# Kernel optimization log

Measured on AMD Instinct MI355X. Metric: run time of the kernel, lower is better.

## Reference

```python
import jax, jax.numpy as jnp
import numpy as np

N, E, D, A = 50000, 800000, 128, 5


def _glorot(key, shape):
    fan = shape[0] + shape[1]
    s = jnp.sqrt(6.0 / fan)
    return jax.random.uniform(key, shape, jnp.float32, -s, s)


def setup_inputs() -> dict:
    key = jax.random.key(0)
    ks = jax.random.split(key, 16)
    x = jax.random.normal(ks[0], (N, D), jnp.float32)
    edge_index = jax.random.randint(ks[1], (2, E), 0, N, jnp.int32)
    return {
        "x": x,
        "anchor_node": _glorot(ks[2], (A, D)),          # NodePromptplus.anchor_prompt
        "attn_w": _glorot(ks[3], (D, A)),               # NodePromptplus.attention (in,out)
        "attn_b": jnp.zeros((A,), jnp.float32),
        "anchor_edge": _glorot(ks[4], (A, D)),          # EdgePromptplus.anchor_prompt
        "w_w": _glorot(ks[5], (2 * D, A)),              # EdgePromptplus.w[0]
        "w_b": jnp.zeros((A,), jnp.float32),
        "cd1_w": _glorot(ks[6], (2 * D, D)),            # causal_discovery Linear1
        "cd1_b": jnp.zeros((D,), jnp.float32),
        "cd2_w": _glorot(ks[7], (D, D)),                # causal_discovery Linear2
        "cd2_b": jnp.zeros((D,), jnp.float32),
        "int_w": _glorot(ks[8], (D, D)),                # intervention Linear
        "int_b": jnp.zeros((D,), jnp.float32),
        "edge_index": edge_index,
        "layer": 0,
    }


def reference(x, anchor_node, attn_w, attn_b, anchor_edge, w_w, w_b,
              cd1_w, cd1_b, cd2_w, cd2_b, int_w, int_b, edge_index, layer):
    # --- NodePromptplus.add ---
    w = jax.nn.softmax(x @ attn_w + attn_b, axis=1)            # [N,A]
    node_px = x + w @ anchor_node                              # [N,D]
    # --- EdgePromptplus.get_prompt ---
    src, dst = edge_index[0], edge_index[1]
    combined_x = jnp.concatenate([x[src], x[dst]], axis=1)     # [E,2D]
    b = jax.nn.softmax(jax.nn.leaky_relu(combined_x @ w_w + w_b), axis=1)  # [E,A]
    edge_prompt = b @ anchor_edge                              # [E,D]
    # --- index_add scatter to both endpoints ---
    agg = jnp.zeros_like(x).at[src].add(edge_prompt).at[dst].add(edge_prompt)
    # --- causal discovery gating + intervention ---
    combined = jnp.concatenate([node_px, agg], axis=1)         # [N,2D]
    h = jax.nn.relu(combined @ cd1_w + cd1_b)
    causal_strength = jax.nn.sigmoid(h @ cd2_w + cd2_b)        # [N,D]
    intervened = (node_px + agg) @ int_w + int_b               # [N,D]
    final_x = node_px + causal_strength * intervened
    return final_x, edge_prompt
```

## Files before the change

### kernel.cpp

```cpp
#include <hip/hip_runtime.h>
#include <math.h>

#define D 128
#define A 5
#define TM 64
#define CSTR 68

__global__ __launch_bounds__(256) void node_prompt_kernel(
    const float* __restrict__ x,
    const float* __restrict__ attn_w, const float* __restrict__ attn_b,
    const float* __restrict__ anchor_node,
    const float* __restrict__ w_w,
    float* __restrict__ node_px,
    float* __restrict__ lsrc, float* __restrict__ ldst, int N)
{
    int t = threadIdx.x;
    int lane = t & 63;
    int j = lane * 2;
    float At0[A], At1[A], AN0[A], AN1[A], Ab[A];
    float W0[A], W1[A], W2[A], W3[A];
    #pragma unroll
    for (int a = 0; a < A; a++) {
        At0[a] = attn_w[(size_t)j * A + a];
        At1[a] = attn_w[(size_t)(j + 1) * A + a];
        AN0[a] = anchor_node[a * D + j];
        AN1[a] = anchor_node[a * D + j + 1];
        Ab[a]  = attn_b[a];
        W0[a]  = w_w[(size_t)j * A + a];
        W1[a]  = w_w[(size_t)(j + 1) * A + a];
        W2[a]  = w_w[(size_t)(D + j) * A + a];
        W3[a]  = w_w[(size_t)(D + j + 1) * A + a];
    }
    int wid = blockIdx.x * 4 + (t >> 6);
    int nw  = gridDim.x * 4;
    for (int n = wid; n < N; n += nw) {
        float2 xv = *(const float2*)&x[(size_t)n * D + j];
        float l[A], es[A], ed[A];
        #pragma unroll
        for (int a = 0; a < A; a++) {
            float p0 = xv.x * At0[a] + xv.y * At1[a];
            float p1 = xv.x * W0[a]  + xv.y * W1[a];
            float p2 = xv.x * W2[a]  + xv.y * W3[a];
            #pragma unroll
            for (int off = 32; off; off >>= 1) {
                p0 += __shfl_xor(p0, off);
                p1 += __shfl_xor(p1, off);
                p2 += __shfl_xor(p2, off);
            }
            l[a]  = p0 + Ab[a];
            es[a] = p1;
            ed[a] = p2;
        }
        float m = l[0];
        #pragma unroll
        for (int a = 1; a < A; a++) m = fmaxf(m, l[a]);
        float s = 0.f;
        #pragma unroll
        for (int a = 0; a < A; a++) { l[a] = __expf(l[a] - m); s += l[a]; }
        float inv = 1.f / s;
        float2 o = xv;
        #pragma unroll
        for (int a = 0; a < A; a++) {
            float w = l[a] * inv;
            o.x += w * AN0[a];
            o.y += w * AN1[a];
        }
        *(float2*)&node_px[(size_t)n * D + j] = o;
        if (lane < A) {
            float vs = es[0], vd = ed[0];
            #pragma unroll
            for (int a = 1; a < A; a++) if (lane == a) { vs = es[a]; vd = ed[a]; }
            lsrc[(size_t)n * A + lane] = vs;
            ldst[(size_t)n * A + lane] = vd;
        }
    }
}

__global__ __launch_bounds__(256) void edge_kernel(
    const int* __restrict__ ei,
    const float* __restrict__ lsrc, const float* __restrict__ ldst,
    const float* __restrict__ w_b, const float* __restrict__ anchor_edge,
    float* __restrict__ edge_prompt, float* __restrict__ bagg, int E)
{
    int t = threadIdx.x;
    int lane = t & 63;
    int j = lane * 2;
    float AE0[A], AE1[A], Wb[A];
    #pragma unroll
    for (int a = 0; a < A; a++) {
        AE0[a] = anchor_edge[a * D + j];
        AE1[a] = anchor_edge[a * D + j + 1];
        Wb[a]  = w_b[a];
    }
    int sub  = lane & 31;
    int half = lane >> 5;
    int wid = blockIdx.x * 4 + (t >> 6);
    int nw  = gridDim.x * 4;
    #pragma unroll 2
    for (int e = wid; e < E; e += nw) {
        int s = __builtin_amdgcn_readfirstlane(ei[e]);
        int d = __builtin_amdgcn_readfirstlane(ei[(size_t)E + e]);
        const float* ps = &lsrc[(size_t)s * A];
        const float* pd = &ldst[(size_t)d * A];
        float l[A];
        #pragma unroll
        for (int a = 0; a < A; a++) {
            float p = ps[a] + pd[a] + Wb[a];
            l[a] = (p > 0.f) ? p : 0.01f * p;
        }
        float m = l[0];
        #pragma unroll
        for (int a = 1; a < A; a++) m = fmaxf(m, l[a]);
        float sum = 0.f;
        #pragma unroll
        for (int a = 0; a < A; a++) { l[a] = __expf(l[a] - m); sum += l[a]; }
        float inv = 1.f / sum;
        float2 ep = make_float2(0.f, 0.f);
        #pragma unroll
        for (int a = 0; a < A; a++) {
            float b = l[a] * inv;
            ep.x += b * AE0[a];
            ep.y += b * AE1[a];
        }
        *(float2*)&edge_prompt[(size_t)e * D + j] = ep;
        if (sub < A) {
            float bv = l[0];
            #pragma unroll
            for (int a = 1; a < A; a++) if (sub == a) bv = l[a];
            bv *= inv;
            int node = half ? d : s;
            atomicAdd(&bagg[(size_t)node * A + sub], bv);
        }
    }
}

__global__ __launch_bounds__(256) void agg_kernel(
    const float* __restrict__ bagg, const float* __restrict__ anchor_edge,
    float* __restrict__ agg, int N)
{
    __shared__ float AE[A * D];
    int t = threadIdx.x;
    for (int f = t; f < A * D; f += 256) AE[f] = anchor_edge[f];
    __syncthreads();
    int total = N * (D / 4);
    for (int i = blockIdx.x * 256 + t; i < total; i += gridDim.x * 256) {
        int n = i >> 5;
        int c = (i & 31) * 4;
        const float* br = &bagg[(size_t)n * A];
        float b0 = br[0], b1 = br[1], b2 = br[2], b3 = br[3], b4 = br[4];
        float4 e0 = *(float4*)&AE[0 * D + c];
        float4 e1 = *(float4*)&AE[1 * D + c];
        float4 e2 = *(float4*)&AE[2 * D + c];
        float4 e3 = *(float4*)&AE[3 * D + c];
        float4 e4 = *(float4*)&AE[4 * D + c];
        float4 r;
        r.x = b0 * e0.x + b1 * e1.x + b2 * e2.x + b3 * e3.x + b4 * e4.x;
        r.y = b0 * e0.y + b1 * e1.y + b2 * e2.y + b3 * e3.y + b4 * e4.y;
        r.z = b0 * e0.z + b1 * e1.z + b2 * e2.z + b3 * e3.z + b4 * e4.z;
        r.w = b0 * e0.w + b1 * e1.w + b2 * e2.w + b3 * e3.w + b4 * e4.w;
        *(float4*)&agg[(size_t)n * D + c] = r;
    }
}

__device__ __forceinline__ void fma4(float4& acc, const float4 cv,
                                     const float4 w0, const float4 w1,
                                     const float4 w2, const float4 w3)
{
    acc.x += cv.x * w0.x + cv.y * w1.x + cv.z * w2.x + cv.w * w3.x;
    acc.y += cv.x * w0.y + cv.y * w1.y + cv.z * w2.y + cv.w * w3.y;
    acc.z += cv.x * w0.z + cv.y * w1.z + cv.z * w2.z + cv.w * w3.z;
    acc.w += cv.x * w0.w + cv.y * w1.w + cv.z * w2.w + cv.w * w3.w;
}

__global__ __launch_bounds__(256) void cd1_kernel(
    const float* __restrict__ node_px, const float* __restrict__ agg,
    const float* __restrict__ cd1_w, const float* __restrict__ cd1_b,
    float* __restrict__ h, int N)
{
    __shared__ float Wt[64 * D];
    __shared__ float Cn[TM * CSTR];
    int t = threadIdx.x;
    int n0 = blockIdx.x * TM;
    int cg = t & 31, ng = t >> 5;
    int c0 = cg * 4;
    float4 acc[8];
    #pragma unroll
    for (int jj = 0; jj < 8; jj++) acc[jj] = make_float4(0.f, 0.f, 0.f, 0.f);

    for (int kt = 0; kt < 4; kt++) {
        int k0 = kt * 64;
        __syncthreads();
        const float4* Wg = (const float4*)(cd1_w + (size_t)k0 * D);
        float4* Wl = (float4*)Wt;
        #pragma unroll
        for (int i = 0; i < 8; i++) Wl[i * 256 + t] = Wg[i * 256 + t];
        const float* src = (k0 < 128) ? node_px : agg;
        int koff = k0 & 127;
        #pragma unroll
        for (int i = 0; i < 4; i++) {
            int f = i * 256 + t;
            int n = f >> 4, k4 = f & 15;
            int nn = n0 + n; if (nn >= N) nn = N - 1;
            float4 v = *(const float4*)&src[(size_t)nn * D + koff + k4 * 4];
            *(float4*)&Cn[n * CSTR + k4 * 4] = v;
        }
        __syncthreads();
        #pragma unroll 4
        for (int k4 = 0; k4 < 16; k4++) {
            float4 w0 = *(float4*)&Wt[(k4 * 4 + 0) * D + c0];
            float4 w1 = *(float4*)&Wt[(k4 * 4 + 1) * D + c0];
            float4 w2 = *(float4*)&Wt[(k4 * 4 + 2) * D + c0];
            float4 w3 = *(float4*)&Wt[(k4 * 4 + 3) * D + c0];
            #pragma unroll
            for (int jj = 0; jj < 8; jj++) {
                float4 cv = *(float4*)&Cn[(ng * 8 + jj) * CSTR + k4 * 4];
                fma4(acc[jj], cv, w0, w1, w2, w3);
            }
        }
    }
    float4 b = *(const float4*)&cd1_b[c0];
    #pragma unroll
    for (int jj = 0; jj < 8; jj++) {
        int n = n0 + ng * 8 + jj;
        if (n < N) {
            float4 r;
            r.x = fmaxf(acc[jj].x + b.x, 0.f);
            r.y = fmaxf(acc[jj].y + b.y, 0.f);
            r.z = fmaxf(acc[jj].z + b.z, 0.f);
            r.w = fmaxf(acc[jj].w + b.w, 0.f);
            *(float4*)&h[(size_t)n * D + c0] = r;
        }
    }
}

__global__ __launch_bounds__(256) void cd2_kernel(
    const float* h_in, const float* __restrict__ cd2_w,
    const float* __restrict__ cd2_b, float* cs_out, int N)
{
    __shared__ float Wt[64 * D];
    __shared__ float Cn[TM * CSTR];
    int t = threadIdx.x;
    int n0 = blockIdx.x * TM;
    int cg = t & 31, ng = t >> 5;
    int c0 = cg * 4;
    float4 acc[8];
    #pragma unroll
    for (int jj = 0; jj < 8; jj++) acc[jj] = make_float4(0.f, 0.f, 0.f, 0.f);

    for (int kt = 0; kt < 2; kt++) {
        int k0 = kt * 64;
        __syncthreads();
        const float4* Wg = (const float4*)(cd2_w + (size_t)k0 * D);
        float4* Wl = (float4*)Wt;
        #pragma unroll
        for (int i = 0; i < 8; i++) Wl[i * 256 + t] = Wg[i * 256 + t];
        #pragma unroll
        for (int i = 0; i < 4; i++) {
            int f = i * 256 + t;
            int n = f >> 4, k4 = f & 15;
            int nn = n0 + n; if (nn >= N) nn = N - 1;
            float4 v = *(const float4*)&h_in[(size_t)nn * D + k0 + k4 * 4];
            *(float4*)&Cn[n * CSTR + k4 * 4] = v;
        }
        __syncthreads();
        #pragma unroll 4
        for (int k4 = 0; k4 < 16; k4++) {
            float4 w0 = *(float4*)&Wt[(k4 * 4 + 0) * D + c0];
            float4 w1 = *(float4*)&Wt[(k4 * 4 + 1) * D + c0];
            float4 w2 = *(float4*)&Wt[(k4 * 4 + 2) * D + c0];
            float4 w3 = *(float4*)&Wt[(k4 * 4 + 3) * D + c0];
            #pragma unroll
            for (int jj = 0; jj < 8; jj++) {
                float4 cv = *(float4*)&Cn[(ng * 8 + jj) * CSTR + k4 * 4];
                fma4(acc[jj], cv, w0, w1, w2, w3);
            }
        }
    }
    float4 b = *(const float4*)&cd2_b[c0];
    #pragma unroll
    for (int jj = 0; jj < 8; jj++) {
        int n = n0 + ng * 8 + jj;
        if (n < N) {
            float4 r;
            r.x = 1.f / (1.f + __expf(-(acc[jj].x + b.x)));
            r.y = 1.f / (1.f + __expf(-(acc[jj].y + b.y)));
            r.z = 1.f / (1.f + __expf(-(acc[jj].z + b.z)));
            r.w = 1.f / (1.f + __expf(-(acc[jj].w + b.w)));
            *(float4*)&cs_out[(size_t)n * D + c0] = r;
        }
    }
}

__global__ __launch_bounds__(256) void final_kernel(
    const float* node_px, const float* __restrict__ agg,
    const float* __restrict__ cs, const float* __restrict__ int_w,
    const float* __restrict__ int_b, float* final_x, int N)
{
    __shared__ float Wt[64 * D];
    __shared__ float Cn[TM * CSTR];
    int t = threadIdx.x;
    int n0 = blockIdx.x * TM;
    int cg = t & 31, ng = t >> 5;
    int c0 = cg * 4;
    float4 acc[8];
    #pragma unroll
    for (int jj = 0; jj < 8; jj++) acc[jj] = make_float4(0.f, 0.f, 0.f, 0.f);

    for (int kt = 0; kt < 2; kt++) {
        int k0 = kt * 64;
        __syncthreads();
        const float4* Wg = (const float4*)(int_w + (size_t)k0 * D);
        float4* Wl = (float4*)Wt;
        #pragma unroll
        for (int i = 0; i < 8; i++) Wl[i * 256 + t] = Wg[i * 256 + t];
        #pragma unroll
        for (int i = 0; i < 4; i++) {
            int f = i * 256 + t;
            int n = f >> 4, k4 = f & 15;
            int nn = n0 + n; if (nn >= N) nn = N - 1;
            float4 a4 = *(const float4*)&node_px[(size_t)nn * D + k0 + k4 * 4];
            float4 b4 = *(const float4*)&agg[(size_t)nn * D + k0 + k4 * 4];
            float4 v = make_float4(a4.x + b4.x, a4.y + b4.y, a4.z + b4.z, a4.w + b4.w);
            *(float4*)&Cn[n * CSTR + k4 * 4] = v;
        }
        __syncthreads();
        #pragma unroll 4
        for (int k4 = 0; k4 < 16; k4++) {
            float4 w0 = *(float4*)&Wt[(k4 * 4 + 0) * D + c0];
            float4 w1 = *(float4*)&Wt[(k4 * 4 + 1) * D + c0];
            float4 w2 = *(float4*)&Wt[(k4 * 4 + 2) * D + c0];
            float4 w3 = *(float4*)&Wt[(k4 * 4 + 3) * D + c0];
            #pragma unroll
            for (int jj = 0; jj < 8; jj++) {
                float4 cv = *(float4*)&Cn[(ng * 8 + jj) * CSTR + k4 * 4];
                fma4(acc[jj], cv, w0, w1, w2, w3);
            }
        }
    }
    float4 b = *(const float4*)&int_b[c0];
    #pragma unroll
    for (int jj = 0; jj < 8; jj++) {
        int n = n0 + ng * 8 + jj;
        if (n < N) {
            float4 iv = make_float4(acc[jj].x + b.x, acc[jj].y + b.y,
                                    acc[jj].z + b.z, acc[jj].w + b.w);
            float4 c4 = *(const float4*)&cs[(size_t)n * D + c0];
            float4 np = *(const float4*)&node_px[(size_t)n * D + c0];
            float4 r;
            r.x = np.x + c4.x * iv.x;
            r.y = np.y + c4.y * iv.y;
            r.z = np.z + c4.z * iv.z;
            r.w = np.w + c4.w * iv.w;
            *(float4*)&final_x[(size_t)n * D + c0] = r;
        }
    }
}

extern "C" void kernel_launch(void* const* d_in, const int* in_sizes, int n_in,
                              void* d_out, int out_size, void* d_ws, size_t ws_size,
                              hipStream_t stream)
{
    const float* x           = (const float*)d_in[0];
    const float* anchor_node = (const float*)d_in[1];
    const float* attn_w      = (const float*)d_in[2];
    const float* attn_b      = (const float*)d_in[3];
    const float* anchor_edge = (const float*)d_in[4];
    const float* w_w         = (const float*)d_in[5];
    const float* w_b         = (const float*)d_in[6];
    const float* cd1_w       = (const float*)d_in[7];
    const float* cd1_b       = (const float*)d_in[8];
    const float* cd2_w       = (const float*)d_in[9];
    const float* cd2_b       = (const float*)d_in[10];
    const float* int_w       = (const float*)d_in[11];
    const float* int_b       = (const float*)d_in[12];
    const int*   ei          = (const int*)d_in[13];

    int N = in_sizes[0] / D;
    int E = in_sizes[13] / 2;

    float* out         = (float*)d_out;
    float* node_px     = out;
    float* edge_prompt = out + (size_t)N * D;
    float* agg         = (float*)d_ws;
    float* h           = agg + (size_t)N * D;
    float* bagg        = h;
    float* lsrc        = h + (size_t)N * A;
    float* ldst        = h + (size_t)2 * N * A;

    hipMemsetAsync(bagg, 0, (size_t)N * A * sizeof(float), stream);

    node_prompt_kernel<<<512, 256, 0, stream>>>(x, attn_w, attn_b, anchor_node, w_w,
                                                node_px, lsrc, ldst, N);
    edge_kernel<<<2048, 256, 0, stream>>>(ei, lsrc, ldst, w_b, anchor_edge,
                                          edge_prompt, bagg, E);
    agg_kernel<<<2048, 256, 0, stream>>>(bagg, anchor_edge, agg, N);

    int nb = (N + TM - 1) / TM;
    cd1_kernel<<<nb, 256, 0, stream>>>(node_px, agg, cd1_w, cd1_b, h, N);
    cd2_kernel<<<nb, 256, 0, stream>>>(h, cd2_w, cd2_b, h, N);
    final_kernel<<<nb, 256, 0, stream>>>(node_px, agg, h, int_w, int_b, node_px, N);
}
```

Measured before the change: 804.8 us.

## Fuse agg, cd1, cd2 and intervention into one tail kernel computing agg on the fly

Replaces the agg kernel and the three dense GEMM kernels with a single fused kernel per 64-node tile. Agg is rebuilt from the 5-wide bagg weights times anchor_edge held in registers, and the hidden activation h stays in shared memory between the cd1 and cd2 stages. The sigmoid gate is kept in registers until the intervention epilogue. This removes the global writes and reads of agg, h and cs and several launches. In exchange it drops the padded shared-memory stride (CSTR 68 becomes an unpadded 128), which may add bank conflicts, and it raises register pressure.

```diff
diff --git a/kernel.cpp b/kernel.cpp
--- a/kernel.cpp
+++ b/kernel.cpp
@@ -4,7 +4,6 @@
 #define D 128
 #define A 5
 #define TM 64
-#define CSTR 68
 
 __global__ __launch_bounds__(256) void node_prompt_kernel(
     const float* __restrict__ x,
@@ -134,34 +133,6 @@
     }
 }
 
-__global__ __launch_bounds__(256) void agg_kernel(
-    const float* __restrict__ bagg, const float* __restrict__ anchor_edge,
-    float* __restrict__ agg, int N)
-{
-    __shared__ float AE[A * D];
-    int t = threadIdx.x;
-    for (int f = t; f < A * D; f += 256) AE[f] = anchor_edge[f];
-    __syncthreads();
-    int total = N * (D / 4);
-    for (int i = blockIdx.x * 256 + t; i < total; i += gridDim.x * 256) {
-        int n = i >> 5;
-        int c = (i & 31) * 4;
-        const float* br = &bagg[(size_t)n * A];
-        float b0 = br[0], b1 = br[1], b2 = br[2], b3 = br[3], b4 = br[4];
-        float4 e0 = *(float4*)&AE[0 * D + c];
-        float4 e1 = *(float4*)&AE[1 * D + c];
-        float4 e2 = *(float4*)&AE[2 * D + c];
-        float4 e3 = *(float4*)&AE[3 * D + c];
-        float4 e4 = *(float4*)&AE[4 * D + c];
-        float4 r;
-        r.x = b0 * e0.x + b1 * e1.x + b2 * e2.x + b3 * e3.x + b4 * e4.x;
-        r.y = b0 * e0.y + b1 * e1.y + b2 * e2.y + b3 * e3.y + b4 * e4.y;
-        r.z = b0 * e0.z + b1 * e1.z + b2 * e2.z + b3 * e3.z + b4 * e4.z;
-        r.w = b0 * e0.w + b1 * e1.w + b2 * e2.w + b3 * e3.w + b4 * e4.w;
-        *(float4*)&agg[(size_t)n * D + c] = r;
-    }
-}
-
 __device__ __forceinline__ void fma4(float4& acc, const float4 cv,
                                      const float4 w0, const float4 w1,
                                      const float4 w2, const float4 w3)
@@ -172,17 +143,41 @@
     acc.w += cv.x * w0.w + cv.y * w1.w + cv.z * w2.w + cv.w * w3.w;
 }
 
-__global__ __launch_bounds__(256) void cd1_kernel(
-    const float* __restrict__ node_px, const float* __restrict__ agg,
+__device__ __forceinline__ float4 agg_otf(const float* __restrict__ br,
+                                          const float4* AEh)
+{
+    float b0 = br[0], b1 = br[1], b2 = br[2], b3 = br[3], b4 = br[4];
+    float4 v;
+    v.x = b0*AEh[0].x + b1*AEh[1].x + b2*AEh[2].x + b3*AEh[3].x + b4*AEh[4].x;
+    v.y = b0*AEh[0].y + b1*AEh[1].y + b2*AEh[2].y + b3*AEh[3].y + b4*AEh[4].y;
+    v.z = b0*AEh[0].z + b1*AEh[1].z + b2*AEh[2].z + b3*AEh[3].z + b4*AEh[4].z;
+    v.w = b0*AEh[0].w + b1*AEh[1].w + b2*AEh[2].w + b3*AEh[3].w + b4*AEh[4].w;
+    return v;
+}
+
+__global__ __launch_bounds__(256) void fused_tail_kernel(
+    const float* __restrict__ node_px, const float* __restrict__ bagg,
+    const float* __restrict__ anchor_edge,
     const float* __restrict__ cd1_w, const float* __restrict__ cd1_b,
-    float* __restrict__ h, int N)
+    const float* __restrict__ cd2_w, const float* __restrict__ cd2_b,
+    const float* __restrict__ int_w, const float* __restrict__ int_b,
+    float* __restrict__ final_x, int N)
 {
     __shared__ float Wt[64 * D];
-    __shared__ float Cn[TM * CSTR];
+    __shared__ float Buf[TM * D];
     int t = threadIdx.x;
     int n0 = blockIdx.x * TM;
     int cg = t & 31, ng = t >> 5;
     int c0 = cg * 4;
+    int k4s = t & 15;
+
+    float4 AEr[2][A];
+    #pragma unroll
+    for (int hh = 0; hh < 2; hh++)
+        #pragma unroll
+        for (int a = 0; a < A; a++)
+            AEr[hh][a] = *(const float4*)&anchor_edge[a * D + hh * 64 + k4s * 4];
+
     float4 acc[8];
     #pragma unroll
     for (int jj = 0; jj < 8; jj++) acc[jj] = make_float4(0.f, 0.f, 0.f, 0.f);
@@ -194,15 +189,18 @@
         float4* Wl = (float4*)Wt;
         #pragma unroll
         for (int i = 0; i < 8; i++) Wl[i * 256 + t] = Wg[i * 256 + t];
-        const float* src = (k0 < 128) ? node_px : agg;
-        int koff = k0 & 127;
         #pragma unroll
         for (int i = 0; i < 4; i++) {
             int f = i * 256 + t;
-            int n = f >> 4, k4 = f & 15;
+            int n = f >> 4;
             int nn = n0 + n; if (nn >= N) nn = N - 1;
-            float4 v = *(const float4*)&src[(size_t)nn * D + koff + k4 * 4];
-            *(float4*)&Cn[n * CSTR + k4 * 4] = v;
+            float4 v;
+            if (kt < 2) {
+                v = *(const float4*)&node_px[(size_t)nn * D + k0 + k4s * 4];
+            } else {
+                v = agg_otf(&bagg[(size_t)nn * A], AEr[kt - 2]);
+            }
+            *(float4*)&Buf[n * D + k4s * 4] = v;
         }
         __syncthreads();
         #pragma unroll 4
@@ -213,40 +211,25 @@
             float4 w3 = *(float4*)&Wt[(k4 * 4 + 3) * D + c0];
             #pragma unroll
             for (int jj = 0; jj < 8; jj++) {
-                float4 cv = *(float4*)&Cn[(ng * 8 + jj) * CSTR + k4 * 4];
+                float4 cv = *(float4*)&Buf[(ng * 8 + jj) * D + k4 * 4];
                 fma4(acc[jj], cv, w0, w1, w2, w3);
             }
         }
     }
-    float4 b = *(const float4*)&cd1_b[c0];
-    #pragma unroll
-    for (int jj = 0; jj < 8; jj++) {
-        int n = n0 + ng * 8 + jj;
-        if (n < N) {
+    {
+        float4 b1v = *(const float4*)&cd1_b[c0];
+        __syncthreads();
+        #pragma unroll
+        for (int jj = 0; jj < 8; jj++) {
             float4 r;
-            r.x = fmaxf(acc[jj].x + b.x, 0.f);
-            r.y = fmaxf(acc[jj].y + b.y, 0.f);
-            r.z = fmaxf(acc[jj].z + b.z, 0.f);
-            r.w = fmaxf(acc[jj].w + b.w, 0.f);
-            *(float4*)&h[(size_t)n * D + c0] = r;
-        }
-    }
-}
-
-__global__ __launch_bounds__(256) void cd2_kernel(
-    const float* h_in, const float* __restrict__ cd2_w,
-    const float* __restrict__ cd2_b, float* cs_out, int N)
-{
-    __shared__ float Wt[64 * D];
-    __shared__ float Cn[TM * CSTR];
-    int t = threadIdx.x;
-    int n0 = blockIdx.x * TM;
-    int cg = t & 31, ng = t >> 5;
-    int c0 = cg * 4;
-    float4 acc[8];
-    #pragma unroll
-    for (int jj = 0; jj < 8; jj++) acc[jj] = make_float4(0.f, 0.f, 0.f, 0.f);
-
+            r.x = fmaxf(acc[jj].x + b1v.x, 0.f);
+            r.y = fmaxf(acc[jj].y + b1v.y, 0.f);
+            r.z = fmaxf(acc[jj].z + b1v.z, 0.f);
+            r.w = fmaxf(acc[jj].w + b1v.w, 0.f);
+            *(float4*)&Buf[(ng * 8 + jj) * D + c0] = r;
+            acc[jj] = make_float4(0.f, 0.f, 0.f, 0.f);
+        }
+    }
     for (int kt = 0; kt < 2; kt++) {
         int k0 = kt * 64;
         __syncthreads();
@@ -254,14 +237,6 @@
         float4* Wl = (float4*)Wt;
         #pragma unroll
         for (int i = 0; i < 8; i++) Wl[i * 256 + t] = Wg[i * 256 + t];
-        #pragma unroll
-        for (int i = 0; i < 4; i++) {
-            int f = i * 256 + t;
-            int n = f >> 4, k4 = f & 15;
-            int nn = n0 + n; if (nn >= N) nn = N - 1;
-            float4 v = *(const float4*)&h_in[(size_t)nn * D + k0 + k4 * 4];
-            *(float4*)&Cn[n * CSTR + k4 * 4] = v;
-        }
         __syncthreads();
         #pragma unroll 4
         for (int k4 = 0; k4 < 16; k4++) {
@@ -271,41 +246,23 @@
             float4 w3 = *(float4*)&Wt[(k4 * 4 + 3) * D + c0];
             #pragma unroll
             for (int jj = 0; jj < 8; jj++) {
-                float4 cv = *(float4*)&Cn[(ng * 8 + jj) * CSTR + k4 * 4];
+                float4 cv = *(float4*)&Buf[(ng * 8 + jj) * D + k0 + k4 * 4];
                 fma4(acc[jj], cv, w0, w1, w2, w3);
             }
         }
     }
-    float4 b = *(const float4*)&cd2_b[c0];
-    #pragma unroll
-    for (int jj = 0; jj < 8; jj++) {
-        int n = n0 + ng * 8 + jj;
-        if (n < N) {
-            float4 r;
-            r.x = 1.f / (1.f + __expf(-(acc[jj].x + b.x)));
-            r.y = 1.f / (1.f + __expf(-(acc[jj].y + b.y)));
-            r.z = 1.f / (1.f + __expf(-(acc[jj].z + b.z)));
-            r.w = 1.f / (1.f + __expf(-(acc[jj].w + b.w)));
-            *(float4*)&cs_out[(size_t)n * D + c0] = r;
-        }
-    }
-}
-
-__global__ __launch_bounds__(256) void final_kernel(
-    const float* node_px, const float* __restrict__ agg,
-    const float* __restrict__ cs, const float* __restrict__ int_w,
-    const float* __restrict__ int_b, float* final_x, int N)
-{
-    __shared__ float Wt[64 * D];
-    __shared__ float Cn[TM * CSTR];
-    int t = threadIdx.x;
-    int n0 = blockIdx.x * TM;
-    int cg = t & 31, ng = t >> 5;
-    int c0 = cg * 4;
-    float4 acc[8];
-    #pragma unroll
-    for (int jj = 0; jj < 8; jj++) acc[jj] = make_float4(0.f, 0.f, 0.f, 0.f);
-
+    float4 cs[8];
+    {
+        float4 b2v = *(const float4*)&cd2_b[c0];
+        #pragma unroll
+        for (int jj = 0; jj < 8; jj++) {
+            cs[jj].x = 1.f / (1.f + __expf(-(acc[jj].x + b2v.x)));
+            cs[jj].y = 1.f / (1.f + __expf(-(acc[jj].y + b2v.y)));
+            cs[jj].z = 1.f / (1.f + __expf(-(acc[jj].z + b2v.z)));
+            cs[jj].w = 1.f / (1.f + __expf(-(acc[jj].w + b2v.w)));
+            acc[jj] = make_float4(0.f, 0.f, 0.f, 0.f);
+        }
+    }
     for (int kt = 0; kt < 2; kt++) {
         int k0 = kt * 64;
         __syncthreads();
@@ -316,12 +273,12 @@
         #pragma unroll
         for (int i = 0; i < 4; i++) {
             int f = i * 256 + t;
-            int n = f >> 4, k4 = f & 15;
+            int n = f >> 4;
             int nn = n0 + n; if (nn >= N) nn = N - 1;
-            float4 a4 = *(const float4*)&node_px[(size_t)nn * D + k0 + k4 * 4];
-            float4 b4 = *(const float4*)&agg[(size_t)nn * D + k0 + k4 * 4];
-            float4 v = make_float4(a4.x + b4.x, a4.y + b4.y, a4.z + b4.z, a4.w + b4.w);
-            *(float4*)&Cn[n * CSTR + k4 * 4] = v;
+            float4 a4 = *(const float4*)&node_px[(size_t)nn * D + k0 + k4s * 4];
+            float4 g4 = agg_otf(&bagg[(size_t)nn * A], AEr[kt]);
+            float4 v = make_float4(a4.x + g4.x, a4.y + g4.y, a4.z + g4.z, a4.w + g4.w);
+            *(float4*)&Buf[n * D + k4s * 4] = v;
         }
         __syncthreads();
         #pragma unroll 4
@@ -332,26 +289,25 @@
             float4 w3 = *(float4*)&Wt[(k4 * 4 + 3) * D + c0];
             #pragma unroll
             for (int jj = 0; jj < 8; jj++) {
-                float4 cv = *(float4*)&Cn[(ng * 8 + jj) * CSTR + k4 * 4];
+                float4 cv = *(float4*)&Buf[(ng * 8 + jj) * D + k4 * 4];
                 fma4(acc[jj], cv, w0, w1, w2, w3);
             }
         }
     }
-    float4 b = *(const float4*)&int_b[c0];
-    #pragma unroll
-    for (int jj = 0; jj < 8; jj++) {
-        int n = n0 + ng * 8 + jj;
-        if (n < N) {
-            float4 iv = make_float4(acc[jj].x + b.x, acc[jj].y + b.y,
-                                    acc[jj].z + b.z, acc[jj].w + b.w);
-            float4 c4 = *(const float4*)&cs[(size_t)n * D + c0];
-            float4 np = *(const float4*)&node_px[(size_t)n * D + c0];
-            float4 r;
-            r.x = np.x + c4.x * iv.x;
-            r.y = np.y + c4.y * iv.y;
-            r.z = np.z + c4.z * iv.z;
-            r.w = np.w + c4.w * iv.w;
-            *(float4*)&final_x[(size_t)n * D + c0] = r;
+    {
+        float4 bi = *(const float4*)&int_b[c0];
+        #pragma unroll
+        for (int jj = 0; jj < 8; jj++) {
+            int n = n0 + ng * 8 + jj;
+            if (n < N) {
+                float4 np = *(const float4*)&node_px[(size_t)n * D + c0];
+                float4 r;
+                r.x = np.x + cs[jj].x * (acc[jj].x + bi.x);
+                r.y = np.y + cs[jj].y * (acc[jj].y + bi.y);
+                r.z = np.z + cs[jj].z * (acc[jj].z + bi.z);
+                r.w = np.w + cs[jj].w * (acc[jj].w + bi.w);
+                *(float4*)&final_x[(size_t)n * D + c0] = r;
+            }
         }
     }
 }
@@ -381,11 +337,9 @@
     float* out         = (float*)d_out;
     float* node_px     = out;
     float* edge_prompt = out + (size_t)N * D;
-    float* agg         = (float*)d_ws;
-    float* h           = agg + (size_t)N * D;
-    float* bagg        = h;
-    float* lsrc        = h + (size_t)N * A;
-    float* ldst        = h + (size_t)2 * N * A;
+    float* bagg        = (float*)d_ws;
+    float* lsrc        = bagg + (size_t)N * A;
+    float* ldst        = bagg + (size_t)2 * N * A;
 
     hipMemsetAsync(bagg, 0, (size_t)N * A * sizeof(float), stream);
 
@@ -393,10 +347,9 @@
                                                 node_px, lsrc, ldst, N);
     edge_kernel<<<2048, 256, 0, stream>>>(ei, lsrc, ldst, w_b, anchor_edge,
                                           edge_prompt, bagg, E);
-    agg_kernel<<<2048, 256, 0, stream>>>(bagg, anchor_edge, agg, N);
 
     int nb = (N + TM - 1) / TM;
-    cd1_kernel<<<nb, 256, 0, stream>>>(node_px, agg, cd1_w, cd1_b, h, N);
-    cd2_kernel<<<nb, 256, 0, stream>>>(h, cd2_w, cd2_b, h, N);
-    final_kernel<<<nb, 256, 0, stream>>>(node_px, agg, h, int_w, int_b, node_px, N);
-}
+    fused_tail_kernel<<<nb, 256, 0, stream>>>(node_px, bagg, anchor_edge,
+                                              cd1_w, cd1_b, cd2_w, cd2_b,
+                                              int_w, int_b, node_px, N);
+}
```

After: 789.1 us. Within noise of the previous version (-1.9%).
